# Kernel optimization log

Measured on AMD Instinct MI355X. Metric: run time of the kernel, lower is better.

Reference implementation:

```python
import jax, jax.numpy as jnp
import numpy as np

N_HEAD = 8
D_MODEL = 512
D_K = 64
D_V = 64
WIN = 1024  # window_size == seq_len (required by posi_att view)
B = 8
LN_EPS = 1e-5


def setup_inputs() -> dict:
    key = jax.random.key(0)
    ks = jax.random.split(key, 12)
    std_qk = np.sqrt(2.0 / (D_MODEL + D_K)).astype(np.float32)
    std_v = np.sqrt(2.0 / (D_MODEL + D_V)).astype(np.float32)
    inp = {
        "q": jax.random.normal(ks[0], (B, WIN, D_MODEL), jnp.float32),
        "k": jax.random.normal(ks[1], (B, WIN, D_MODEL), jnp.float32),
        "v": jax.random.normal(ks[2], (B, WIN, D_MODEL), jnp.float32),
        # Linear weights stored torch-style: [out_features, in_features]
        "wq_W": jax.random.normal(ks[3], (N_HEAD * D_K, D_MODEL), jnp.float32) * std_qk,
        "wq_b": jnp.zeros((N_HEAD * D_K,), jnp.float32),
        "wk_W": jax.random.normal(ks[4], (N_HEAD * D_K, D_MODEL), jnp.float32) * std_qk,
        "wk_b": jnp.zeros((N_HEAD * D_K,), jnp.float32),
        "wv_W": jax.random.normal(ks[5], (N_HEAD * D_V, D_MODEL), jnp.float32) * std_v,
        "wv_b": jnp.zeros((N_HEAD * D_V,), jnp.float32),
        "fc_W": jax.random.normal(ks[6], (D_MODEL, N_HEAD * D_V), jnp.float32)
        * np.sqrt(2.0 / (D_MODEL + N_HEAD * D_V)).astype(np.float32),
        "fc_b": jnp.zeros((D_MODEL,), jnp.float32),
        "ln_g": jnp.ones((D_MODEL,), jnp.float32),
        "ln_b": jnp.zeros((D_MODEL,), jnp.float32),
        "p0": jnp.ones((N_HEAD,), jnp.float32),
        "p1": jnp.ones((N_HEAD,), jnp.float32),
        "p2": jnp.ones((N_HEAD,), jnp.float32) * 0.5,
        "p3": jnp.zeros((N_HEAD,), jnp.float32),
    }
    return inp


def _posi_att(p0, p1, p2, p3):
    idx = jnp.arange(WIN, dtype=jnp.float32)
    scale = jnp.abs(idx[:, None] - idx[None, :])          # |i-j|, [L,L]
    asyn = (idx[:, None] < idx[None, :]).astype(jnp.float32)  # 1 if i<j
    sp1 = jax.nn.softplus(p1)[:, None, None]
    sp2 = jax.nn.softplus(p2)[:, None, None]
    s = scale[None]
    return p0[:, None, None] * (
        jnp.exp(-sp1 * s) + jnp.exp(-sp2 * s) + p3[:, None, None] * asyn[None]
    )  # [H, L, L]


def reference(q, k, v, wq_W, wq_b, wk_W, wk_b, wv_W, wv_b, fc_W, fc_b,
              ln_g, ln_b, p0, p1, p2, p3):
    residual = q
    # projections -> [B, L, H, D]
    qh = (q @ wq_W.T + wq_b).reshape(B, WIN, N_HEAD, D_K)
    kh = (k @ wk_W.T + wk_b).reshape(B, WIN, N_HEAD, D_K)
    vh = (v @ wv_W.T + wv_b).reshape(B, WIN, N_HEAD, D_V)
    temperature = jnp.sqrt(jnp.float32(D_K))
    # scores: [H, B, Lq, Lk]
    attn = jnp.einsum("bqhd,bkhd->hbqk", qh, kh) / temperature
    posi = _posi_att(p0, p1, p2, p3)  # [H, Lk, Lk]
    attn = jax.nn.softmax(attn + posi[:, None], axis=-1)
    out = jnp.einsum("hbqk,bkhd->bqhd", attn, vh).reshape(B, WIN, N_HEAD * D_V)
    out = out @ fc_W.T + fc_b  # dropout = identity (eval)
    out = out + residual
    mu = jnp.mean(out, axis=-1, keepdims=True)
    var = jnp.var(out, axis=-1, keepdims=True)
    out = (out - mu) / jnp.sqrt(var + LN_EPS) * ln_g + ln_b
    return out, attn.reshape(N_HEAD * B, WIN, WIN)
```

## Files before the change

kernel.cpp:

```cpp
#include <hip/hip_runtime.h>
#include <math.h>


typedef __attribute__((ext_vector_type(4))) float f32x4;
typedef __attribute__((ext_vector_type(8))) __bf16 bf8;
typedef __attribute__((ext_vector_type(8))) unsigned short us8;
typedef __attribute__((ext_vector_type(4))) unsigned short us4;

#define LOG2E 1.44269504088896f

static __device__ __forceinline__ unsigned short f2bf(float f) {
  union { float f; unsigned u; } x; x.f = f;
  unsigned r = x.u + 0x7fffu + ((x.u >> 16) & 1u);
  return (unsigned short)(r >> 16);
}

static __device__ __forceinline__ float bf2f(unsigned short u) {
  union { unsigned u; float f; } x; x.u = ((unsigned)u) << 16;
  return x.f;
}

static __device__ __forceinline__ f32x4 mfma16(bf8 a, bf8 b, f32x4 c) {
  return __builtin_amdgcn_mfma_f32_16x16x32_bf16(a, b, c, 0, 0, 0);
}

__global__ void posi_build(const float* __restrict__ p0, const float* __restrict__ p1,
                           const float* __restrict__ p2, const float* __restrict__ p3,
                           float* __restrict__ tab) {
  int idx = blockIdx.x * 256 + threadIdx.x;
  if (idx >= 8 * 2048) return;
  int h = idx >> 11, dd = idx & 2047;
  if (dd >= 2047) { tab[idx] = 0.f; return; }
  float d = (float)(dd - 1023);
  float s = fabsf(d);
  float a1 = p1[h], a2 = p2[h];
  float sp1 = (a1 > 20.f) ? a1 : log1pf(expf(a1));
  float sp2 = (a2 > 20.f) ? a2 : log1pf(expf(a2));
  float asyn = (d < 0.f) ? 1.f : 0.f;
  tab[idx] = p0[h] * (expf(-sp1 * s) + expf(-sp2 * s) + p3[h] * asyn) * LOG2E;
}

__global__ __launch_bounds__(256) void qkv_proj(
    const float* __restrict__ q, const float* __restrict__ k, const float* __restrict__ v,
    const float* __restrict__ wqW, const float* __restrict__ wkW, const float* __restrict__ wvW,
    const float* __restrict__ wqb, const float* __restrict__ wkb, const float* __restrict__ wvb,
    unsigned short* __restrict__ QH, unsigned short* __restrict__ KH,
    unsigned short* __restrict__ VT) {
  __shared__ __align__(16) unsigned short As[128 * 32];
  __shared__ __align__(16) unsigned short Bs[128 * 32];
  const int tid = threadIdx.x;
  const int lane = tid & 63, w = tid >> 6;
  const int lg = lane >> 4, ln = lane & 15;
  const int wr = w >> 1, wc = w & 1;
  const int bm = blockIdx.x, bn = blockIdx.y, z = blockIdx.z;

  const float* A    = (z == 0) ? q   : (z == 1) ? k   : v;
  const float* W    = (z == 0) ? wqW : (z == 1) ? wkW : wvW;
  const float* bias = (z == 0) ? wqb : (z == 1) ? wkb : wvb;
  unsigned short* outb = (z == 0) ? QH : (z == 1) ? KH : VT;
  const float scale = (z == 0) ? 0.125f * LOG2E : 1.f;

  f32x4 acc[4][4] = {};

  for (int kt = 0; kt < 16; ++kt) {
    const int k0 = kt * 32;
    f32x4 areg[4]; f32x4 breg[4];
#pragma unroll
    for (int i = 0; i < 4; ++i) {
      int e = i * 1024 + tid * 4;
      int r = e >> 5, c = e & 31;
      areg[i] = *(const f32x4*)(A + (size_t)(bm * 128 + r) * 512 + k0 + c);
      breg[i] = *(const f32x4*)(W + (size_t)(bn * 128 + r) * 512 + k0 + c);
    }
    __syncthreads();
#pragma unroll
    for (int i = 0; i < 4; ++i) {
      int e = i * 1024 + tid * 4;
      int r = e >> 5, c = e & 31;
      us4 ua, ub;
#pragma unroll
      for (int t = 0; t < 4; ++t) { ua[t] = f2bf(areg[i][t]); ub[t] = f2bf(breg[i][t]); }
      *(us4*)&As[r * 32 + c] = ua;
      *(us4*)&Bs[r * 32 + c] = ub;
    }
    __syncthreads();
    bf8 af[4], bfm[4];
#pragma unroll
    for (int m = 0; m < 4; ++m)
      af[m] = *(const bf8*)&As[(wr * 64 + m * 16 + ln) * 32 + lg * 8];
#pragma unroll
    for (int n = 0; n < 4; ++n)
      bfm[n] = *(const bf8*)&Bs[(wc * 64 + n * 16 + ln) * 32 + lg * 8];
#pragma unroll
    for (int m = 0; m < 4; ++m)
#pragma unroll
      for (int n = 0; n < 4; ++n)
        acc[m][n] = mfma16(af[m], bfm[n], acc[m][n]);
  }

#pragma unroll
  for (int m = 0; m < 4; ++m) {
#pragma unroll
    for (int n = 0; n < 4; ++n) {
      const int col = bn * 128 + wc * 64 + n * 16 + ln;
      const int row0 = bm * 128 + wr * 64 + m * 16 + lg * 4;
      const float bcol = bias[col];
#pragma unroll
      for (int r = 0; r < 4; ++r) {
        const int rg = row0 + r;
        const float val = (acc[m][n][r] + bcol) * scale;
        const int bb = rg >> 10, lq = rg & 1023, hh = col >> 6, dd = col & 63;
        if (z < 2)
          outb[((size_t)(bb * 8 + hh) * 1024 + lq) * 64 + dd] = f2bf(val);
        else
          outb[((size_t)(bb * 8 + hh) * 64 + dd) * 1024 + lq] = f2bf(val);
      }
    }
  }
}

__global__ __launch_bounds__(256) void gemm_fc(
    const unsigned short* __restrict__ Ap, const float* __restrict__ W,
    const float* __restrict__ bias, const float* __restrict__ resid,
    float* __restrict__ outf) {
  __shared__ __align__(16) unsigned short As[128 * 32];
  __shared__ __align__(16) unsigned short Bs[128 * 32];
  const int tid = threadIdx.x;
  const int lane = tid & 63, w = tid >> 6;
  const int lg = lane >> 4, ln = lane & 15;
  const int wr = w >> 1, wc = w & 1;
  const int bm = blockIdx.x, bn = blockIdx.y;

  f32x4 acc[4][4] = {};

  for (int kt = 0; kt < 16; ++kt) {
    const int k0 = kt * 32;
    us8 areg16[2]; f32x4 breg[4];
#pragma unroll
    for (int i = 0; i < 2; ++i) {
      int ch = i * 256 + tid;
      int r = ch >> 2, c = (ch & 3) * 8;
      areg16[i] = *(const us8*)(Ap + (size_t)(bm * 128 + r) * 512 + k0 + c);
    }
#pragma unroll
    for (int i = 0; i < 4; ++i) {
      int e = i * 1024 + tid * 4;
      int r = e >> 5, c = e & 31;
      breg[i] = *(const f32x4*)(W + (size_t)(bn * 128 + r) * 512 + k0 + c);
    }
    __syncthreads();
#pragma unroll
    for (int i = 0; i < 2; ++i) {
      int ch = i * 256 + tid;
      int r = ch >> 2, c = (ch & 3) * 8;
      *(us8*)&As[r * 32 + c] = areg16[i];
    }
#pragma unroll
    for (int i = 0; i < 4; ++i) {
      int e = i * 1024 + tid * 4;
      int r = e >> 5, c = e & 31;
      us4 u;
#pragma unroll
      for (int t = 0; t < 4; ++t) u[t] = f2bf(breg[i][t]);
      *(us4*)&Bs[r * 32 + c] = u;
    }
    __syncthreads();
    bf8 af[4], bfm[4];
#pragma unroll
    for (int m = 0; m < 4; ++m)
      af[m] = *(const bf8*)&As[(wr * 64 + m * 16 + ln) * 32 + lg * 8];
#pragma unroll
    for (int n = 0; n < 4; ++n)
      bfm[n] = *(const bf8*)&Bs[(wc * 64 + n * 16 + ln) * 32 + lg * 8];
#pragma unroll
    for (int m = 0; m < 4; ++m)
#pragma unroll
      for (int n = 0; n < 4; ++n)
        acc[m][n] = mfma16(af[m], bfm[n], acc[m][n]);
  }

#pragma unroll
  for (int m = 0; m < 4; ++m) {
#pragma unroll
    for (int n = 0; n < 4; ++n) {
      const int col = bn * 128 + wc * 64 + n * 16 + ln;
      const int row0 = bm * 128 + wr * 64 + m * 16 + lg * 4;
      const float bcol = bias[col];
#pragma unroll
      for (int r = 0; r < 4; ++r) {
        const int rg = row0 + r;
        outf[(size_t)rg * 512 + col] =
            acc[m][n][r] + bcol + resid[(size_t)rg * 512 + col];
      }
    }
  }
}

__global__ __launch_bounds__(512, 4) void attn_fused(
    const unsigned short* __restrict__ QH, const unsigned short* __restrict__ KH,
    const unsigned short* __restrict__ VT, const float* __restrict__ posi_tab,
    float* __restrict__ attn_out, unsigned short* __restrict__ Omat) {
  __shared__ __align__(16) unsigned short pbuf[2][16][1048];
  __shared__ float posi_w[1056];
  __shared__ float lred[2][4][16];

  const int tid = threadIdx.x;
  const int lane = tid & 63, w = tid >> 6;
  const int lg = lane >> 4, ln = lane & 15;
  const int sp = w >> 2, kq = w & 3;
  const int wgid = blockIdx.x;
  const int bh = wgid & 63, qblk = wgid >> 6;
  const int b = bh >> 3, h = bh & 7;
  const int q0 = qblk * 32;

  for (int i = tid; i < 1056; i += 512) posi_w[i] = posi_tab[h * 2048 + q0 + i];
  __syncthreads();

  const size_t base = (size_t)(b * 8 + h) * 1024 * 64;
  const unsigned short* Qb = QH + base;
  const unsigned short* Kb = KH + base;
  const unsigned short* Vb = VT + base;

  const int qrow = sp * 16 + ln;
  const unsigned short* qr = Qb + (size_t)(q0 + qrow) * 64 + lg * 8;
  const bf8 bq0 = *(const bf8*)qr;
  const bf8 bq1 = *(const bf8*)(qr + 32);

  const int kbase = kq << 8;
  f32x4 laccv = {0.f, 0.f, 0.f, 0.f};
#pragma unroll
  for (int kt = 0; kt < 4; ++kt) {
    const int k0 = kbase + kt * 64;
    bf8 ka[4][2];
#pragma unroll
    for (int n = 0; n < 4; ++n) {
      const unsigned short* kr = Kb + (size_t)(k0 + n * 16 + ln) * 64 + lg * 8;
      ka[n][0] = *(const bf8*)kr;
      ka[n][1] = *(const bf8*)(kr + 32);
    }
#pragma unroll
    for (int n = 0; n < 4; ++n) {
      f32x4 sc = {};
      sc = mfma16(ka[n][0], bq0, sc);
      sc = mfma16(ka[n][1], bq1, sc);
      const int kjb = k0 + n * 16 + lg * 4;
      const int pli = qrow - kjb + 1023;
      us4 pb;
#pragma unroll
      for (int r = 0; r < 4; ++r) {
        float p = exp2f(sc[r] + posi_w[pli - r]);
        laccv[r] += p;
        pb[r] = f2bf(p);
      }
      *(us4*)&pbuf[sp][ln][kjb] = pb;
    }
  }
  float lacc = laccv[0] + laccv[1] + laccv[2] + laccv[3];
  lacc += __shfl_xor(lacc, 16, 64);
  lacc += __shfl_xor(lacc, 32, 64);
  if (lg == 0) lred[sp][kq][ln] = lacc;

  const unsigned short* vrow = Vb + (size_t)(kq * 16 + ln) * 1024;
  bf8 va[4][2];
#pragma unroll
  for (int j = 0; j < 4; ++j) {
    va[j][0] = *(const bf8*)(vrow + j * 64 + lg * 8);
    va[j][1] = *(const bf8*)(vrow + j * 64 + 32 + lg * 8);
  }

  __syncthreads();

  float rl[16];
#pragma unroll
  for (int r = 0; r < 16; ++r)
    rl[r] = 1.f / (lred[sp][0][r] + lred[sp][1][r] +
                   lred[sp][2][r] + lred[sp][3][r]);

  f32x4 oacc = {};
  float* abb = attn_out + (size_t)(h * 8 + b) * 1024 * 1024;
#pragma unroll
  for (int g = 0; g < 4; ++g) {
    bf8 vn[4][2];
    if (g < 3) {
#pragma unroll
      for (int j = 0; j < 4; ++j) {
        const int k0 = (g + 1) * 256 + j * 64;
        vn[j][0] = *(const bf8*)(vrow + k0 + lg * 8);
        vn[j][1] = *(const bf8*)(vrow + k0 + 32 + lg * 8);
      }
    }
#pragma unroll
    for (int j = 0; j < 4; ++j) {
      const int kt = g * 4 + j;
      const int k0 = kt * 64;
      const bf8 pa0 = *(const bf8*)&pbuf[sp][ln][k0 + lg * 8];
      const bf8 pa1 = *(const bf8*)&pbuf[sp][ln][k0 + 32 + lg * 8];
      oacc = mfma16(pa0, va[j][0], oacc);
      oacc = mfma16(pa1, va[j][1], oacc);
      us4 pv = *(const us4*)&pbuf[sp][kt][kq * 256 + lane * 4];
      f32x4 f0;
#pragma unroll
      for (int t = 0; t < 4; ++t) f0[t] = bf2f(pv[t]) * rl[kt];
      __builtin_nontemporal_store(
          f0, (f32x4*)(abb + (size_t)(q0 + sp * 16 + kt) * 1024 + kq * 256 + lane * 4));
    }
#pragma unroll
    for (int j = 0; j < 4; ++j) { va[j][0] = vn[j][0]; va[j][1] = vn[j][1]; }
  }

#pragma unroll
  for (int r = 0; r < 4; ++r) {
    const int row = lg * 4 + r;
    Omat[(size_t)(b * 1024 + q0 + sp * 16 + row) * 512 +
         h * 64 + kq * 16 + ln] = f2bf(oacc[r] * rl[row]);
  }
}

__global__ __launch_bounds__(256) void ln_fused(const float* __restrict__ x,
                                                const float* __restrict__ g,
                                                const float* __restrict__ bb,
                                                float* __restrict__ out) {
  const int lane = threadIdx.x & 63, w = threadIdx.x >> 6;
  const size_t row = (size_t)blockIdx.x * 4 + w;
  const float* xr = x + row * 512;
  f32x4 v0 = *(const f32x4*)(xr + lane * 8);
  f32x4 v1 = *(const f32x4*)(xr + lane * 8 + 4);
  float s = v0[0] + v0[1] + v0[2] + v0[3] + v1[0] + v1[1] + v1[2] + v1[3];
  float sq = v0[0] * v0[0] + v0[1] * v0[1] + v0[2] * v0[2] + v0[3] * v0[3] +
             v1[0] * v1[0] + v1[1] * v1[1] + v1[2] * v1[2] + v1[3] * v1[3];
#pragma unroll
  for (int msk = 1; msk <= 32; msk <<= 1) {
    s += __shfl_xor(s, msk, 64);
    sq += __shfl_xor(sq, msk, 64);
  }
  const float mu = s * (1.f / 512.f);
  const float var = sq * (1.f / 512.f) - mu * mu;
  const float rs = rsqrtf(var + 1e-5f);
  f32x4 g0 = *(const f32x4*)(g + lane * 8), g1 = *(const f32x4*)(g + lane * 8 + 4);
  f32x4 b0 = *(const f32x4*)(bb + lane * 8), b1 = *(const f32x4*)(bb + lane * 8 + 4);
  f32x4 o0, o1;
#pragma unroll
  for (int j = 0; j < 4; ++j) {
    o0[j] = (v0[j] - mu) * rs * g0[j] + b0[j];
    o1[j] = (v1[j] - mu) * rs * g1[j] + b1[j];
  }
  *(f32x4*)(out + row * 512 + lane * 8) = o0;
  *(f32x4*)(out + row * 512 + lane * 8 + 4) = o1;
}

extern "C" void kernel_launch(void* const* d_in, const int* in_sizes, int n_in,
                              void* d_out, int out_size, void* d_ws, size_t ws_size,
                              hipStream_t stream) {
  const float* q   = (const float*)d_in[0];
  const float* k   = (const float*)d_in[1];
  const float* v   = (const float*)d_in[2];
  const float* wqW = (const float*)d_in[3];
  const float* wqb = (const float*)d_in[4];
  const float* wkW = (const float*)d_in[5];
  const float* wkb = (const float*)d_in[6];
  const float* wvW = (const float*)d_in[7];
  const float* wvb = (const float*)d_in[8];
  const float* fcW = (const float*)d_in[9];
  const float* fcb = (const float*)d_in[10];
  const float* lng = (const float*)d_in[11];
  const float* lnb = (const float*)d_in[12];
  const float* p0  = (const float*)d_in[13];
  const float* p1  = (const float*)d_in[14];
  const float* p2  = (const float*)d_in[15];
  const float* p3  = (const float*)d_in[16];

  char* ws = (char*)d_ws;
  unsigned short* QH   = (unsigned short*)(ws);
  unsigned short* KH   = (unsigned short*)(ws + 8388608);
  unsigned short* VT   = (unsigned short*)(ws + 16777216);
  unsigned short* Omat = (unsigned short*)(ws + 25165824);
  float* posi          = (float*)(ws + 33554432);
  float* preln         = (float*)(ws + 33619968);

  float* out0 = (float*)d_out;
  float* attn = out0 + (size_t)8 * 1024 * 512;

  posi_build<<<64, 256, 0, stream>>>(p0, p1, p2, p3, posi);
  qkv_proj<<<dim3(64, 4, 3), 256, 0, stream>>>(q, k, v, wqW, wkW, wvW,
                                               wqb, wkb, wvb, QH, KH, VT);
  attn_fused<<<2048, 512, 0, stream>>>(QH, KH, VT, posi, attn, Omat);
  gemm_fc<<<dim3(64, 4), 256, 0, stream>>>(Omat, fcW, fcb, q, preln);
  ln_fused<<<2048, 256, 0, stream>>>(preln, lng, lnb, out0);
}
```

Before: 198.9 us.

## Fuse positional bias into attention and LayerNorm into output projection GEMM

Drops the separate posi_build kernel by computing each block's positional-bias window inside attn_fused, from the per-head parameters. Replaces gemm_fc and ln_fused with one kernel. Each block computes full 512-column rows for 32 rows, then reduces mean and variance in shared memory and writes the normalized output directly. This removes two launches and the round trip of the pre-LN buffer through global memory. In exchange, every block of the fused GEMM re-reads and converts the entire fc weight matrix, and the fused GEMM has only 256 blocks, which may lower efficiency.

```diff
diff --git a/kernel.cpp b/kernel.cpp
--- a/kernel.cpp
+++ b/kernel.cpp
@@ -22,22 +22,6 @@
 
 static __device__ __forceinline__ f32x4 mfma16(bf8 a, bf8 b, f32x4 c) {
   return __builtin_amdgcn_mfma_f32_16x16x32_bf16(a, b, c, 0, 0, 0);
-}
-
-__global__ void posi_build(const float* __restrict__ p0, const float* __restrict__ p1,
-                           const float* __restrict__ p2, const float* __restrict__ p3,
-                           float* __restrict__ tab) {
-  int idx = blockIdx.x * 256 + threadIdx.x;
-  if (idx >= 8 * 2048) return;
-  int h = idx >> 11, dd = idx & 2047;
-  if (dd >= 2047) { tab[idx] = 0.f; return; }
-  float d = (float)(dd - 1023);
-  float s = fabsf(d);
-  float a1 = p1[h], a2 = p2[h];
-  float sp1 = (a1 > 20.f) ? a1 : log1pf(expf(a1));
-  float sp2 = (a2 > 20.f) ? a2 : log1pf(expf(a2));
-  float asyn = (d < 0.f) ? 1.f : 0.f;
-  tab[idx] = p0[h] * (expf(-sp1 * s) + expf(-sp2 * s) + p3[h] * asyn) * LOG2E;
 }
 
 __global__ __launch_bounds__(256) void qkv_proj(
@@ -119,86 +103,11 @@
   }
 }
 
-__global__ __launch_bounds__(256) void gemm_fc(
-    const unsigned short* __restrict__ Ap, const float* __restrict__ W,
-    const float* __restrict__ bias, const float* __restrict__ resid,
-    float* __restrict__ outf) {
-  __shared__ __align__(16) unsigned short As[128 * 32];
-  __shared__ __align__(16) unsigned short Bs[128 * 32];
-  const int tid = threadIdx.x;
-  const int lane = tid & 63, w = tid >> 6;
-  const int lg = lane >> 4, ln = lane & 15;
-  const int wr = w >> 1, wc = w & 1;
-  const int bm = blockIdx.x, bn = blockIdx.y;
-
-  f32x4 acc[4][4] = {};
-
-  for (int kt = 0; kt < 16; ++kt) {
-    const int k0 = kt * 32;
-    us8 areg16[2]; f32x4 breg[4];
-#pragma unroll
-    for (int i = 0; i < 2; ++i) {
-      int ch = i * 256 + tid;
-      int r = ch >> 2, c = (ch & 3) * 8;
-      areg16[i] = *(const us8*)(Ap + (size_t)(bm * 128 + r) * 512 + k0 + c);
-    }
-#pragma unroll
-    for (int i = 0; i < 4; ++i) {
-      int e = i * 1024 + tid * 4;
-      int r = e >> 5, c = e & 31;
-      breg[i] = *(const f32x4*)(W + (size_t)(bn * 128 + r) * 512 + k0 + c);
-    }
-    __syncthreads();
-#pragma unroll
-    for (int i = 0; i < 2; ++i) {
-      int ch = i * 256 + tid;
-      int r = ch >> 2, c = (ch & 3) * 8;
-      *(us8*)&As[r * 32 + c] = areg16[i];
-    }
-#pragma unroll
-    for (int i = 0; i < 4; ++i) {
-      int e = i * 1024 + tid * 4;
-      int r = e >> 5, c = e & 31;
-      us4 u;
-#pragma unroll
-      for (int t = 0; t < 4; ++t) u[t] = f2bf(breg[i][t]);
-      *(us4*)&Bs[r * 32 + c] = u;
-    }
-    __syncthreads();
-    bf8 af[4], bfm[4];
-#pragma unroll
-    for (int m = 0; m < 4; ++m)
-      af[m] = *(const bf8*)&As[(wr * 64 + m * 16 + ln) * 32 + lg * 8];
-#pragma unroll
-    for (int n = 0; n < 4; ++n)
-      bfm[n] = *(const bf8*)&Bs[(wc * 64 + n * 16 + ln) * 32 + lg * 8];
-#pragma unroll
-    for (int m = 0; m < 4; ++m)
-#pragma unroll
-      for (int n = 0; n < 4; ++n)
-        acc[m][n] = mfma16(af[m], bfm[n], acc[m][n]);
-  }
-
-#pragma unroll
-  for (int m = 0; m < 4; ++m) {
-#pragma unroll
-    for (int n = 0; n < 4; ++n) {
-      const int col = bn * 128 + wc * 64 + n * 16 + ln;
-      const int row0 = bm * 128 + wr * 64 + m * 16 + lg * 4;
-      const float bcol = bias[col];
-#pragma unroll
-      for (int r = 0; r < 4; ++r) {
-        const int rg = row0 + r;
-        outf[(size_t)rg * 512 + col] =
-            acc[m][n][r] + bcol + resid[(size_t)rg * 512 + col];
-      }
-    }
-  }
-}
-
 __global__ __launch_bounds__(512, 4) void attn_fused(
     const unsigned short* __restrict__ QH, const unsigned short* __restrict__ KH,
-    const unsigned short* __restrict__ VT, const float* __restrict__ posi_tab,
+    const unsigned short* __restrict__ VT,
+    const float* __restrict__ p0, const float* __restrict__ p1,
+    const float* __restrict__ p2, const float* __restrict__ p3,
     float* __restrict__ attn_out, unsigned short* __restrict__ Omat) {
   __shared__ __align__(16) unsigned short pbuf[2][16][1048];
   __shared__ float posi_w[1056];
@@ -213,7 +122,17 @@
   const int b = bh >> 3, h = bh & 7;
   const int q0 = qblk * 32;
 
-  for (int i = tid; i < 1056; i += 512) posi_w[i] = posi_tab[h * 2048 + q0 + i];
+  {
+    const float p0h = p0[h], p1h = p1[h], p2h = p2[h], p3h = p3[h];
+    const float sp1 = (p1h > 20.f) ? p1h : log1pf(expf(p1h));
+    const float sp2 = (p2h > 20.f) ? p2h : log1pf(expf(p2h));
+    for (int i = tid; i < 1056; i += 512) {
+      const float d = (float)(q0 + i - 1023);
+      const float s = fabsf(d);
+      posi_w[i] = p0h * (expf(-sp1 * s) + expf(-sp2 * s) +
+                         ((d < 0.f) ? p3h : 0.f)) * LOG2E;
+    }
+  }
   __syncthreads();
 
   const size_t base = (size_t)(b * 8 + h) * 1024 * 64;
@@ -316,36 +235,109 @@
   }
 }
 
-__global__ __launch_bounds__(256) void ln_fused(const float* __restrict__ x,
-                                                const float* __restrict__ g,
-                                                const float* __restrict__ bb,
-                                                float* __restrict__ out) {
-  const int lane = threadIdx.x & 63, w = threadIdx.x >> 6;
-  const size_t row = (size_t)blockIdx.x * 4 + w;
-  const float* xr = x + row * 512;
-  f32x4 v0 = *(const f32x4*)(xr + lane * 8);
-  f32x4 v1 = *(const f32x4*)(xr + lane * 8 + 4);
-  float s = v0[0] + v0[1] + v0[2] + v0[3] + v1[0] + v1[1] + v1[2] + v1[3];
-  float sq = v0[0] * v0[0] + v0[1] * v0[1] + v0[2] * v0[2] + v0[3] * v0[3] +
-             v1[0] * v1[0] + v1[1] * v1[1] + v1[2] * v1[2] + v1[3] * v1[3];
-#pragma unroll
-  for (int msk = 1; msk <= 32; msk <<= 1) {
-    s += __shfl_xor(s, msk, 64);
-    sq += __shfl_xor(sq, msk, 64);
-  }
-  const float mu = s * (1.f / 512.f);
-  const float var = sq * (1.f / 512.f) - mu * mu;
-  const float rs = rsqrtf(var + 1e-5f);
-  f32x4 g0 = *(const f32x4*)(g + lane * 8), g1 = *(const f32x4*)(g + lane * 8 + 4);
-  f32x4 b0 = *(const f32x4*)(bb + lane * 8), b1 = *(const f32x4*)(bb + lane * 8 + 4);
-  f32x4 o0, o1;
-#pragma unroll
-  for (int j = 0; j < 4; ++j) {
-    o0[j] = (v0[j] - mu) * rs * g0[j] + b0[j];
-    o1[j] = (v1[j] - mu) * rs * g1[j] + b1[j];
-  }
-  *(f32x4*)(out + row * 512 + lane * 8) = o0;
-  *(f32x4*)(out + row * 512 + lane * 8 + 4) = o1;
+__global__ __launch_bounds__(512, 4) void gemm_fc_ln(
+    const unsigned short* __restrict__ Ap, const float* __restrict__ W,
+    const float* __restrict__ bias, const float* __restrict__ resid,
+    const float* __restrict__ lng, const float* __restrict__ lnb,
+    float* __restrict__ out) {
+  __shared__ __align__(16) unsigned short As[32 * 32];
+  __shared__ __align__(16) unsigned short Bs[512 * 32];
+  __shared__ float lsum[4][32], lsq[4][32];
+  __shared__ float murs[32][2];
+
+  const int tid = threadIdx.x;
+  const int lane = tid & 63, w = tid >> 6;
+  const int lg = lane >> 4, ln = lane & 15;
+  const int mh = w & 1, nc = w >> 1;
+  const int bm = blockIdx.x;
+
+  f32x4 acc[8] = {};
+
+  for (int kt = 0; kt < 16; ++kt) {
+    const int k0 = kt * 32;
+    us8 areg; f32x4 breg[8];
+    if (tid < 128) {
+      int r = tid >> 2, c8 = (tid & 3) * 8;
+      areg = *(const us8*)(Ap + (size_t)(bm * 32 + r) * 512 + k0 + c8);
+    }
+#pragma unroll
+    for (int i = 0; i < 8; ++i) {
+      int e = i * 2048 + tid * 4;
+      int r = e >> 5, c = e & 31;
+      breg[i] = *(const f32x4*)(W + (size_t)r * 512 + k0 + c);
+    }
+    __syncthreads();
+    if (tid < 128) {
+      int r = tid >> 2, c8 = (tid & 3) * 8;
+      *(us8*)&As[r * 32 + c8] = areg;
+    }
+#pragma unroll
+    for (int i = 0; i < 8; ++i) {
+      int e = i * 2048 + tid * 4;
+      int r = e >> 5, c = e & 31;
+      us4 u;
+#pragma unroll
+      for (int t = 0; t < 4; ++t) u[t] = f2bf(breg[i][t]);
+      *(us4*)&Bs[r * 32 + c] = u;
+    }
+    __syncthreads();
+    const bf8 af = *(const bf8*)&As[(mh * 16 + ln) * 32 + lg * 8];
+#pragma unroll
+    for (int nf = 0; nf < 8; ++nf) {
+      const bf8 bf = *(const bf8*)&Bs[(nc * 128 + nf * 16 + ln) * 32 + lg * 8];
+      acc[nf] = mfma16(af, bf, acc[nf]);
+    }
+  }
+
+  float bcol[8];
+#pragma unroll
+  for (int nf = 0; nf < 8; ++nf) bcol[nf] = bias[nc * 128 + nf * 16 + ln];
+#pragma unroll
+  for (int nf = 0; nf < 8; ++nf) {
+    const int col = nc * 128 + nf * 16 + ln;
+#pragma unroll
+    for (int r = 0; r < 4; ++r) {
+      const int rg = bm * 32 + mh * 16 + lg * 4 + r;
+      acc[nf][r] += bcol[nf] + resid[(size_t)rg * 512 + col];
+    }
+  }
+#pragma unroll
+  for (int r = 0; r < 4; ++r) {
+    float ps = 0.f, pq = 0.f;
+#pragma unroll
+    for (int nf = 0; nf < 8; ++nf) { ps += acc[nf][r]; pq += acc[nf][r] * acc[nf][r]; }
+#pragma unroll
+    for (int msk = 1; msk <= 8; msk <<= 1) {
+      ps += __shfl_xor(ps, msk, 64);
+      pq += __shfl_xor(pq, msk, 64);
+    }
+    if (ln == 0) {
+      lsum[nc][mh * 16 + lg * 4 + r] = ps;
+      lsq[nc][mh * 16 + lg * 4 + r] = pq;
+    }
+  }
+  __syncthreads();
+  if (tid < 32) {
+    const float s = lsum[0][tid] + lsum[1][tid] + lsum[2][tid] + lsum[3][tid];
+    const float q = lsq[0][tid] + lsq[1][tid] + lsq[2][tid] + lsq[3][tid];
+    const float mu = s * (1.f / 512.f);
+    const float var = q * (1.f / 512.f) - mu * mu;
+    murs[tid][0] = mu;
+    murs[tid][1] = rsqrtf(var + 1e-5f);
+  }
+  __syncthreads();
+#pragma unroll
+  for (int nf = 0; nf < 8; ++nf) {
+    const int col = nc * 128 + nf * 16 + ln;
+    const float gc = lng[col], bc = lnb[col];
+#pragma unroll
+    for (int r = 0; r < 4; ++r) {
+      const int tr = mh * 16 + lg * 4 + r;
+      const int rg = bm * 32 + tr;
+      out[(size_t)rg * 512 + col] =
+          (acc[nf][r] - murs[tr][0]) * murs[tr][1] * gc + bc;
+    }
+  }
 }
 
 extern "C" void kernel_launch(void* const* d_in, const int* in_sizes, int n_in,
@@ -374,16 +366,12 @@
   unsigned short* KH   = (unsigned short*)(ws + 8388608);
   unsigned short* VT   = (unsigned short*)(ws + 16777216);
   unsigned short* Omat = (unsigned short*)(ws + 25165824);
-  float* posi          = (float*)(ws + 33554432);
-  float* preln         = (float*)(ws + 33619968);
 
   float* out0 = (float*)d_out;
   float* attn = out0 + (size_t)8 * 1024 * 512;
 
-  posi_build<<<64, 256, 0, stream>>>(p0, p1, p2, p3, posi);
   qkv_proj<<<dim3(64, 4, 3), 256, 0, stream>>>(q, k, v, wqW, wkW, wvW,
                                                wqb, wkb, wvb, QH, KH, VT);
-  attn_fused<<<2048, 512, 0, stream>>>(QH, KH, VT, posi, attn, Omat);
-  gemm_fc<<<dim3(64, 4), 256, 0, stream>>>(Omat, fcW, fcb, q, preln);
-  ln_fused<<<2048, 256, 0, stream>>>(preln, lng, lnb, out0);
-}
+  attn_fused<<<2048, 512, 0, stream>>>(QH, KH, VT, p0, p1, p2, p3, attn, Omat);
+  gemm_fc_ln<<<256, 512, 0, stream>>>(Omat, fcW, fcb, q, lng, lnb, out0);
+}
```

Measured after the change: 195.8 us (median of 3 runs). No clear change (-1.5%).
